# Performance work log

Measured on AMD Instinct MI355X. Metric: run time of the kernel, lower is better.

The kernel has to match this reference:

```python
import jax, jax.numpy as jnp
import numpy as np

NEGATIVE = 5
MORPH_VOCAB = 200002  # morph_size + 2 (pad + extra row)
D = 128
B = 32768
M = 6


def setup_inputs() -> dict:
    key = jax.random.key(0)
    k = jax.random.split(key, 7)
    data = jax.random.randint(k[0], (B, 2 + 2 * NEGATIVE), 0, 2, dtype=jnp.int64 if jax.config.jax_enable_x64 else jnp.int32)
    word2morph = jax.random.randint(k[1], (B, M), 0, 200000)
    word2morph_mask = jax.random.uniform(k[2], (B, M, 1), dtype=jnp.float32)
    ctx2morph = jax.random.randint(k[3], (B, 1 + NEGATIVE, M), 0, 200000)
    ctx2morph_mask = jax.random.uniform(k[4], (B, 1 + NEGATIVE, M, 1), dtype=jnp.float32)
    # learned tables; torch inits emb0 ~ U(-0.5/D, 0.5/D) and emb1 = 0;
    # use small random values so the reference exercises nontrivial math
    emb0 = jax.random.uniform(k[5], (MORPH_VOCAB, D), minval=-0.5 / D, maxval=0.5 / D, dtype=jnp.float32)
    emb1 = jax.random.uniform(k[6], (MORPH_VOCAB, D), minval=-0.5 / D, maxval=0.5 / D, dtype=jnp.float32)
    return {
        "data": data,
        "word2morph": word2morph,
        "word2morph_mask": word2morph_mask,
        "ctx2morph": ctx2morph,
        "ctx2morph_mask": ctx2morph_mask,
        "emb0": emb0,
        "emb1": emb1,
    }


def reference(data, word2morph, word2morph_mask, ctx2morph, ctx2morph_mask, emb0, emb1):
    neg_mask = data[:, 2 + NEGATIVE:].astype(jnp.float32)              # [B, neg]
    # masked embedding-bag sums over morphemes
    w_embs = jnp.sum(emb0[word2morph] * word2morph_mask, axis=1)        # [B, D]
    c_embs = jnp.sum(emb1[ctx2morph[:, 0]] * ctx2morph_mask[:, 0], axis=1)  # [B, D]
    n_embs = jnp.sum(emb1[ctx2morph[:, 1:1 + NEGATIVE]] * ctx2morph_mask[:, 1:1 + NEGATIVE], axis=2)  # [B, neg, D]
    # dot-product scores
    pos_ips = jnp.sum(w_embs * c_embs, axis=1)                          # [B]
    neg_ips = jnp.einsum("bnd,bd->bn", n_embs, w_embs)                 # [B, neg]
    # clamped logsigmoid losses
    pos_loss = jnp.sum(-jax.nn.log_sigmoid(jnp.clip(pos_ips, -10.0, 10.0)))
    neg_loss = jnp.sum(-jax.nn.log_sigmoid(jnp.clip(-neg_ips, -10.0, 10.0)) * neg_mask)
    return pos_loss + neg_loss
```

## Files before the change

### kernel.cpp

```cpp
#include <hip/hip_runtime.h>

#define NEG 5
#define MM 6
#define NCTX 6
#define DD 128
#define WPB 4
#define RPW 2
#define RPB (WPB * RPW)
#define DROW 12

#define SB() __builtin_amdgcn_sched_barrier(0)

__device__ __forceinline__ int geti(const int4& v, int c) {
    switch (c) { case 0: return v.x; case 1: return v.y; case 2: return v.z; default: return v.w; }
}
__device__ __forceinline__ float getf(const float4& v, int c) {
    switch (c) { case 0: return v.x; case 1: return v.y; case 2: return v.z; default: return v.w; }
}

template<int J>
__device__ __forceinline__ void issue_ctx(float4* dst, const int4& ci, int base,
                                          const float* __restrict__ emb1, int d0) {
    #pragma unroll
    for (int m = 0; m < MM; ++m) {
        const int flat = J * MM + m;
        const int k = flat >> 2, c = flat & 3;
        const int idx = __shfl(geti(ci, c), base + k, 64);
        dst[m] = *reinterpret_cast<const float4*>(emb1 + (size_t)idx * DD + d0);
    }
}

template<int J>
__device__ __forceinline__ float consume_ctx(const float4* src, const float4& cmk,
                                             int base, const float4& w) {
    float ex = 0.f, ey = 0.f, ez = 0.f, ew = 0.f;
    #pragma unroll
    for (int m = 0; m < MM; ++m) {
        const int flat = J * MM + m;
        const int k = flat >> 2, c = flat & 3;
        const float mk = __shfl(getf(cmk, c), base + 9 + k, 64);
        ex += src[m].x * mk; ey += src[m].y * mk;
        ez += src[m].z * mk; ew += src[m].w * mk;
    }
    return w.x * ex + w.y * ey + w.z * ez + w.w * ew;
}

__global__ __launch_bounds__(256) void sg_loss_kernel(
    const int*   __restrict__ data,
    const int*   __restrict__ w2m,
    const float* __restrict__ w2m_mask,
    const int*   __restrict__ c2m,
    const float* __restrict__ c2m_mask,
    const float* __restrict__ emb0,
    const float* __restrict__ emb1,
    float*       __restrict__ out,
    int B)
{
    const int lane  = threadIdx.x & 63;
    const int wid   = threadIdx.x >> 6;
    const int sub   = lane >> 5;
    const int slane = lane & 31;
    const int base  = lane & 32;
    const int b     = blockIdx.x * RPB + wid * RPW + sub;

    float loss = 0.0f;

    if (b < B) {
        int4   ci  = {0, 0, 0, 0};
        float4 cmk = {0.f, 0.f, 0.f, 0.f};
        int    wi  = 0;
        float  wmk = 0.f;
        int    nm  = 0;

        if (slane < 9) {
            ci  = reinterpret_cast<const int4*>(c2m + (size_t)b * (NCTX * MM))[slane];
        } else if (slane < 18) {
            cmk = reinterpret_cast<const float4*>(c2m_mask + (size_t)b * (NCTX * MM))[slane - 9];
        } else if (slane < 24) {
            wi  = w2m[(size_t)b * MM + (slane - 18)];
        } else if (slane < 30) {
            wmk = w2m_mask[(size_t)b * MM + (slane - 24)];
        }
        if (slane < NEG) nm = data[(size_t)b * DROW + 2 + NEG + slane];

        float nmf[NEG];
        #pragma unroll
        for (int n = 0; n < NEG; ++n)
            nmf[n] = (float)__shfl(nm, base + n, 64);

        const int d0 = slane * 4;

        float4 wr[MM];
        #pragma unroll
        for (int m = 0; m < MM; ++m) {
            const int idx = __shfl(wi, base + 18 + m, 64);
            wr[m] = *reinterpret_cast<const float4*>(emb0 + (size_t)idx * DD + d0);
        }
        float4 A[MM], Bv[MM], C[MM];
        issue_ctx<0>(A,  ci, base, emb1, d0);
        issue_ctx<1>(Bv, ci, base, emb1, d0);
        SB();

        float4 w = {0.f, 0.f, 0.f, 0.f};
        #pragma unroll
        for (int m = 0; m < MM; ++m) {
            const float mk = __shfl(wmk, base + 24 + m, 64);
            w.x += wr[m].x * mk; w.y += wr[m].y * mk;
            w.z += wr[m].z * mk; w.w += wr[m].w * mk;
        }
        issue_ctx<2>(C, ci, base, emb1, d0);
        SB();

        float p[NCTX];
        p[0] = consume_ctx<0>(A,  cmk, base, w);  issue_ctx<3>(A,  ci, base, emb1, d0); SB();
        p[1] = consume_ctx<1>(Bv, cmk, base, w);  issue_ctx<4>(Bv, ci, base, emb1, d0); SB();
        p[2] = consume_ctx<2>(C,  cmk, base, w);  issue_ctx<5>(C,  ci, base, emb1, d0); SB();
        p[3] = consume_ctx<3>(A,  cmk, base, w);
        p[4] = consume_ctx<4>(Bv, cmk, base, w);
        p[5] = consume_ctx<5>(C,  cmk, base, w);

        #pragma unroll
        for (int j = 0; j < NCTX; ++j) {
            float v = p[j];
            #pragma unroll
            for (int off = 16; off >= 1; off >>= 1)
                v += __shfl_xor(v, off, 64);
            p[j] = v;
        }

        if (slane == 0) {
            float x = fminf(fmaxf(p[0], -10.0f), 10.0f);
            loss = log1pf(expf(-x));
            #pragma unroll
            for (int n = 0; n < NEG; ++n) {
                float y = fminf(fmaxf(-p[1 + n], -10.0f), 10.0f);
                loss += log1pf(expf(-y)) * nmf[n];
            }
        }
    }

    __shared__ float sacc[RPB];
    if (slane == 0) sacc[wid * RPW + sub] = loss;
    __syncthreads();
    if (threadIdx.x == 0) {
        float s = 0.0f;
        #pragma unroll
        for (int i = 0; i < RPB; ++i) s += sacc[i];
        atomicAdd(out, s);
    }
}

extern "C" void kernel_launch(void* const* d_in, const int* in_sizes, int n_in,
                              void* d_out, int out_size, void* d_ws, size_t ws_size,
                              hipStream_t stream) {
    const int*   data     = (const int*)  d_in[0];
    const int*   w2m      = (const int*)  d_in[1];
    const float* w2m_mask = (const float*)d_in[2];
    const int*   c2m      = (const int*)  d_in[3];
    const float* c2m_mask = (const float*)d_in[4];
    const float* emb0     = (const float*)d_in[5];
    const float* emb1     = (const float*)d_in[6];
    float* out = (float*)d_out;

    const int B = in_sizes[1] / MM;

    hipMemsetAsync(out, 0, sizeof(float), stream);

    const int blocks = (B + RPB - 1) / RPB;
    sg_loss_kernel<<<blocks, 64 * WPB, 0, stream>>>(
        data, w2m, w2m_mask, c2m, c2m_mask, emb0, emb1, out, B);
}
```

Measured before the change: 109.9 us.

## Split word-embedding bag into separate kernel staged through workspace

Computes the masked word embedding sums in a first kernel and writes them to a workspace buffer, then a second kernel gathers context/negative embeddings, reads the precomputed word vector and forms the dot products and loss. It also restructures the per-context dot to fold the mask after a per-morph dot. The aim is to lower register pressure and let all three context gather batches issue up front; it adds a full B×D round trip through memory and an extra launch. The fused kernel is kept as a fallback when workspace is too small.

```diff
diff --git a/kernel.cpp b/kernel.cpp
--- a/kernel.cpp
+++ b/kernel.cpp
@@ -18,6 +18,42 @@
     switch (c) { case 0: return v.x; case 1: return v.y; case 2: return v.z; default: return v.w; }
 }
 
+__global__ __launch_bounds__(256) void sg_w_kernel(
+    const int*   __restrict__ w2m,
+    const float* __restrict__ w2m_mask,
+    const float* __restrict__ emb0,
+    float*       __restrict__ wbuf,
+    int B)
+{
+    const int lane  = threadIdx.x & 63;
+    const int wid   = threadIdx.x >> 6;
+    const int sub   = lane >> 5;
+    const int slane = lane & 31;
+    const int base  = lane & 32;
+    const int b     = blockIdx.x * RPB + wid * RPW + sub;
+    if (b >= B) return;
+
+    int wi = 0; float wmk = 0.f;
+    if (slane < MM)           wi  = w2m[(size_t)b * MM + slane];
+    else if (slane < 2 * MM)  wmk = w2m_mask[(size_t)b * MM + (slane - MM)];
+
+    const int d0 = slane * 4;
+    float4 rr[MM]; float mk[MM];
+    #pragma unroll
+    for (int m = 0; m < MM; ++m) {
+        const int idx = __shfl(wi, base + m, 64);
+        mk[m]         = __shfl(wmk, base + MM + m, 64);
+        rr[m] = *reinterpret_cast<const float4*>(emb0 + (size_t)idx * DD + d0);
+    }
+    float4 acc = {0.f, 0.f, 0.f, 0.f};
+    #pragma unroll
+    for (int m = 0; m < MM; ++m) {
+        acc.x += rr[m].x * mk[m]; acc.y += rr[m].y * mk[m];
+        acc.z += rr[m].z * mk[m]; acc.w += rr[m].w * mk[m];
+    }
+    *reinterpret_cast<float4*>(wbuf + (size_t)b * DD + d0) = acc;
+}
+
 template<int J>
 __device__ __forceinline__ void issue_ctx(float4* dst, const int4& ci, int base,
                                           const float* __restrict__ emb1, int d0) {
@@ -31,21 +67,99 @@
 }
 
 template<int J>
-__device__ __forceinline__ float consume_ctx(const float4* src, const float4& cmk,
+__device__ __forceinline__ float consume_dot(const float4* src, const float4& cmk,
                                              int base, const float4& w) {
-    float ex = 0.f, ey = 0.f, ez = 0.f, ew = 0.f;
+    float pj = 0.f;
     #pragma unroll
     for (int m = 0; m < MM; ++m) {
         const int flat = J * MM + m;
         const int k = flat >> 2, c = flat & 3;
         const float mk = __shfl(getf(cmk, c), base + 9 + k, 64);
-        ex += src[m].x * mk; ey += src[m].y * mk;
-        ez += src[m].z * mk; ew += src[m].w * mk;
-    }
-    return w.x * ex + w.y * ey + w.z * ez + w.w * ew;
-}
-
-__global__ __launch_bounds__(256) void sg_loss_kernel(
+        pj += mk * (src[m].x * w.x + src[m].y * w.y + src[m].z * w.z + src[m].w * w.w);
+    }
+    return pj;
+}
+
+__global__ __launch_bounds__(256) void sg_dot_kernel(
+    const int*   __restrict__ data,
+    const int*   __restrict__ c2m,
+    const float* __restrict__ c2m_mask,
+    const float* __restrict__ emb1,
+    const float* __restrict__ wbuf,
+    float*       __restrict__ out,
+    int B)
+{
+    const int lane  = threadIdx.x & 63;
+    const int wid   = threadIdx.x >> 6;
+    const int sub   = lane >> 5;
+    const int slane = lane & 31;
+    const int base  = lane & 32;
+    const int b     = blockIdx.x * RPB + wid * RPW + sub;
+
+    float loss = 0.0f;
+
+    if (b < B) {
+        int4   ci  = {0, 0, 0, 0};
+        float4 cmk = {0.f, 0.f, 0.f, 0.f};
+        int    nm  = 0;
+        if (slane < 9)       ci  = reinterpret_cast<const int4*>(c2m + (size_t)b * 36)[slane];
+        else if (slane < 18) cmk = reinterpret_cast<const float4*>(c2m_mask + (size_t)b * 36)[slane - 9];
+        if (slane < NEG)     nm  = data[(size_t)b * DROW + 2 + NEG + slane];
+
+        float nmf[NEG];
+        #pragma unroll
+        for (int n = 0; n < NEG; ++n)
+            nmf[n] = (float)__shfl(nm, base + n, 64);
+
+        const int d0 = slane * 4;
+        const float4 w = *reinterpret_cast<const float4*>(wbuf + (size_t)b * DD + d0);
+
+        float4 A[MM], Bv[MM], C[MM];
+        issue_ctx<0>(A,  ci, base, emb1, d0);
+        issue_ctx<1>(Bv, ci, base, emb1, d0);
+        issue_ctx<2>(C,  ci, base, emb1, d0);
+        SB();
+
+        float p[NCTX];
+        p[0] = consume_dot<0>(A,  cmk, base, w);  issue_ctx<3>(A,  ci, base, emb1, d0); SB();
+        p[1] = consume_dot<1>(Bv, cmk, base, w);  issue_ctx<4>(Bv, ci, base, emb1, d0); SB();
+        p[2] = consume_dot<2>(C,  cmk, base, w);  issue_ctx<5>(C,  ci, base, emb1, d0); SB();
+        p[3] = consume_dot<3>(A,  cmk, base, w);
+        p[4] = consume_dot<4>(Bv, cmk, base, w);
+        p[5] = consume_dot<5>(C,  cmk, base, w);
+
+        #pragma unroll
+        for (int j = 0; j < NCTX; ++j) {
+            float v = p[j];
+            #pragma unroll
+            for (int off = 16; off >= 1; off >>= 1)
+                v += __shfl_xor(v, off, 64);
+            p[j] = v;
+        }
+
+        if (slane == 0) {
+            float x = fminf(fmaxf(p[0], -10.0f), 10.0f);
+            loss = log1pf(expf(-x));
+            #pragma unroll
+            for (int n = 0; n < NEG; ++n) {
+                float y = fminf(fmaxf(-p[1 + n], -10.0f), 10.0f);
+                loss += log1pf(expf(-y)) * nmf[n];
+            }
+        }
+    }
+
+    __shared__ float sacc[RPB];
+    if (slane == 0) sacc[wid * RPW + sub] = loss;
+    __syncthreads();
+    if (threadIdx.x == 0) {
+        float s = 0.0f;
+        #pragma unroll
+        for (int i = 0; i < RPB; ++i) s += sacc[i];
+        atomicAdd(out, s);
+    }
+}
+
+__global__ __launch_bounds__(256) void sg_fused_kernel(
     const int*   __restrict__ data,
     const int*   __restrict__ w2m,
     const float* __restrict__ w2m_mask,
@@ -64,32 +178,20 @@
     const int b     = blockIdx.x * RPB + wid * RPW + sub;
 
     float loss = 0.0f;
-
     if (b < B) {
-        int4   ci  = {0, 0, 0, 0};
-        float4 cmk = {0.f, 0.f, 0.f, 0.f};
-        int    wi  = 0;
-        float  wmk = 0.f;
-        int    nm  = 0;
-
-        if (slane < 9) {
-            ci  = reinterpret_cast<const int4*>(c2m + (size_t)b * (NCTX * MM))[slane];
-        } else if (slane < 18) {
-            cmk = reinterpret_cast<const float4*>(c2m_mask + (size_t)b * (NCTX * MM))[slane - 9];
-        } else if (slane < 24) {
-            wi  = w2m[(size_t)b * MM + (slane - 18)];
-        } else if (slane < 30) {
-            wmk = w2m_mask[(size_t)b * MM + (slane - 24)];
-        }
+        int4 ci = {0,0,0,0}; float4 cmk = {0.f,0.f,0.f,0.f};
+        int wi = 0; float wmk = 0.f; int nm = 0;
+        if (slane < 9)       ci  = reinterpret_cast<const int4*>(c2m + (size_t)b * 36)[slane];
+        else if (slane < 18) cmk = reinterpret_cast<const float4*>(c2m_mask + (size_t)b * 36)[slane - 9];
+        else if (slane < 24) wi  = w2m[(size_t)b * MM + (slane - 18)];
+        else if (slane < 30) wmk = w2m_mask[(size_t)b * MM + (slane - 24)];
         if (slane < NEG) nm = data[(size_t)b * DROW + 2 + NEG + slane];
 
         float nmf[NEG];
         #pragma unroll
-        for (int n = 0; n < NEG; ++n)
-            nmf[n] = (float)__shfl(nm, base + n, 64);
+        for (int n = 0; n < NEG; ++n) nmf[n] = (float)__shfl(nm, base + n, 64);
 
         const int d0 = slane * 4;
-
         float4 wr[MM];
         #pragma unroll
         for (int m = 0; m < MM; ++m) {
@@ -97,11 +199,10 @@
             wr[m] = *reinterpret_cast<const float4*>(emb0 + (size_t)idx * DD + d0);
         }
         float4 A[MM], Bv[MM], C[MM];
-        issue_ctx<0>(A,  ci, base, emb1, d0);
+        issue_ctx<0>(A, ci, base, emb1, d0);
         issue_ctx<1>(Bv, ci, base, emb1, d0);
         SB();
-
-        float4 w = {0.f, 0.f, 0.f, 0.f};
+        float4 w = {0.f,0.f,0.f,0.f};
         #pragma unroll
         for (int m = 0; m < MM; ++m) {
             const float mk = __shfl(wmk, base + 24 + m, 64);
@@ -110,24 +211,21 @@
         }
         issue_ctx<2>(C, ci, base, emb1, d0);
         SB();
-
         float p[NCTX];
-        p[0] = consume_ctx<0>(A,  cmk, base, w);  issue_ctx<3>(A,  ci, base, emb1, d0); SB();
-        p[1] = consume_ctx<1>(Bv, cmk, base, w);  issue_ctx<4>(Bv, ci, base, emb1, d0); SB();
-        p[2] = consume_ctx<2>(C,  cmk, base, w);  issue_ctx<5>(C,  ci, base, emb1, d0); SB();
-        p[3] = consume_ctx<3>(A,  cmk, base, w);
-        p[4] = consume_ctx<4>(Bv, cmk, base, w);
-        p[5] = consume_ctx<5>(C,  cmk, base, w);
+        p[0] = consume_dot<0>(A,  cmk, base, w);  issue_ctx<3>(A,  ci, base, emb1, d0); SB();
+        p[1] = consume_dot<1>(Bv, cmk, base, w);  issue_ctx<4>(Bv, ci, base, emb1, d0); SB();
+        p[2] = consume_dot<2>(C,  cmk, base, w);  issue_ctx<5>(C,  ci, base, emb1, d0); SB();
+        p[3] = consume_dot<3>(A,  cmk, base, w);
+        p[4] = consume_dot<4>(Bv, cmk, base, w);
+        p[5] = consume_dot<5>(C,  cmk, base, w);
 
         #pragma unroll
         for (int j = 0; j < NCTX; ++j) {
             float v = p[j];
             #pragma unroll
-            for (int off = 16; off >= 1; off >>= 1)
-                v += __shfl_xor(v, off, 64);
+            for (int off = 16; off >= 1; off >>= 1) v += __shfl_xor(v, off, 64);
             p[j] = v;
         }
-
         if (slane == 0) {
             float x = fminf(fmaxf(p[0], -10.0f), 10.0f);
             loss = log1pf(expf(-x));
@@ -138,7 +236,6 @@
             }
         }
     }
-
     __shared__ float sacc[RPB];
     if (slane == 0) sacc[wid * RPW + sub] = loss;
     __syncthreads();
@@ -163,10 +260,17 @@
     float* out = (float*)d_out;
 
     const int B = in_sizes[1] / MM;
+    const int blocks = (B + RPB - 1) / RPB;
 
     hipMemsetAsync(out, 0, sizeof(float), stream);
 
-    const int blocks = (B + RPB - 1) / RPB;
-    sg_loss_kernel<<<blocks, 64 * WPB, 0, stream>>>(
-        data, w2m, w2m_mask, c2m, c2m_mask, emb0, emb1, out, B);
-}
+    const size_t need = (size_t)B * DD * sizeof(float);
+    if (ws_size >= need) {
+        float* wbuf = (float*)d_ws;
+        sg_w_kernel<<<blocks, 64 * WPB, 0, stream>>>(w2m, w2m_mask, emb0, wbuf, B);
+        sg_dot_kernel<<<blocks, 64 * WPB, 0, stream>>>(data, c2m, c2m_mask, emb1, wbuf, out, B);
+    } else {
+        sg_fused_kernel<<<blocks, 64 * WPB, 0, stream>>>(
+            data, w2m, w2m_mask, c2m, c2m_mask, emb0, emb1, out, B);
+    }
+}
```

New measurement: 118.1 us. +7.4%, slower.
